# Kernel optimization log

Hardware: AMD Instinct MI355X
Metric: run time of the kernel (lower is better)

Reference implementation:

```python
import jax, jax.numpy as jnp
import numpy as np

BN_EPS = 1e-5


def _gather_neighbors(feat, idx):
    # feat: [B, N, C]; idx: [B, N, K] -> [B, N, K, C]
    B, N, C = feat.shape
    K = idx.shape[-1]
    g = jnp.take_along_axis(feat, idx.reshape(B, N * K)[:, :, None], axis=1)
    return g.reshape(B, N, K, C)


def setup_inputs() -> dict:
    key = jax.random.key(0)
    k1, k2, k3 = jax.random.split(key, 3)
    B, C, N, K, Cout = 4, 128, 4096, 16, 256
    x = jax.random.normal(k1, (B, C, N, 1), dtype=jnp.float32)
    edge_index = jax.random.randint(k2, (2, B, N, K), 0, N, dtype=jnp.int64)
    # 1x1 conv weight [Cout, 2C] (kaiming-like scale), bias zeros (per reset_parameters)
    fan_in = 2 * C
    w = jax.random.normal(k3, (Cout, 2 * C), dtype=jnp.float32) * np.sqrt(2.0 / fan_in)
    b = jnp.zeros((Cout,), dtype=jnp.float32)
    gamma = jnp.ones((Cout,), dtype=jnp.float32)
    beta = jnp.zeros((Cout,), dtype=jnp.float32)
    return {"x": x, "w": w, "b": b, "gamma": gamma, "beta": beta,
            "edge_index": edge_index}


def reference(x, w, b, gamma, beta, edge_index):
    # x: [B, C, N, 1], edge_index: [2, B, N, K]
    B, C, N, _ = x.shape
    feat = jnp.transpose(x[:, :, :, 0], (0, 2, 1))            # [B, N, C]
    x_i = _gather_neighbors(feat, edge_index[1])              # [B, N, K, C]
    x_j = _gather_neighbors(feat, edge_index[0])              # [B, N, K, C]
    h = jnp.concatenate([x_i, x_j - x_i], axis=-1)            # [B, N, K, 2C]
    # 1x1 conv == per-position matmul
    y = jnp.einsum('bnkc,oc->bnko', h, w) + b                 # [B, N, K, Cout]
    y = jax.nn.relu(y)
    # BatchNorm2d (train mode): biased stats over (B, N, K) per channel
    mean = jnp.mean(y, axis=(0, 1, 2))
    var = jnp.mean(jnp.square(y), axis=(0, 1, 2)) - jnp.square(mean)
    y = (y - mean) * jax.lax.rsqrt(var + BN_EPS) * gamma + beta
    # max over neighbors K, keepdim on last torch dim
    out = jnp.max(y, axis=2)                                  # [B, N, Cout]
    return jnp.transpose(out, (0, 2, 1))[:, :, :, None]       # [B, Cout, N, 1]
```

## Files before the change

### kernel.cpp

```cpp
#include <hip/hip_runtime.h>
#include <hip/hip_bf16.h>

#define BB 4
#define CC 128
#define TWOC 256
#define NN 4096
#define KK 16
#define COUT 256
#define BNK (BB*NN*KK)
#define NODES (BB*NN)

typedef __attribute__((ext_vector_type(8))) short short8;
typedef __attribute__((ext_vector_type(4))) float f32x4;

static __device__ __forceinline__ unsigned short f2bs(float f) {
  union { __hip_bfloat16 h; unsigned short s; } u;
  u.h = __float2bfloat16(f);
  return u.s;
}
static __device__ __forceinline__ float bs2f(unsigned short s) {
  union { unsigned int u; float f; } v;
  v.u = ((unsigned int)s) << 16;
  return v.f;
}

__global__ void __launch_bounds__(256) k0_prep(const float* __restrict__ x,
                                               unsigned short* __restrict__ featbf,
                                               const float* __restrict__ w,
                                               unsigned short* __restrict__ w12,
                                               float* __restrict__ gsum,
                                               float* __restrict__ gsq) {
  __shared__ float tile[64][129];
  int b = blockIdx.x >> 6;
  int n0 = (blockIdx.x & 63) << 6;
  int t = threadIdx.x;
  if (blockIdx.x == 0) { gsum[t] = 0.f; gsq[t] = 0.f; }
  {
    int flat = blockIdx.x * 256 + t;
    int col = flat >> 7, k = flat & 127;
    float v = (col < COUT) ? (w[col * TWOC + k] - w[col * TWOC + CC + k])
                           : w[(col - COUT) * TWOC + CC + k];
    w12[flat] = f2bs(v);
  }
#pragma unroll
  for (int i = 0; i < 32; ++i) {
    int flat = t + i * 256;
    int c = flat >> 6;
    int nl = flat & 63;
    tile[nl][c] = x[((size_t)(b * CC + c) * NN) + n0 + nl];
  }
  __syncthreads();
#pragma unroll
  for (int i = 0; i < 8; ++i) {
    int e = t + i * 256;
    int c4 = (e & 31) << 2;
    int nl = e >> 5;
    ushort4 u;
    u.x = f2bs(tile[nl][c4 + 0]);
    u.y = f2bs(tile[nl][c4 + 1]);
    u.z = f2bs(tile[nl][c4 + 2]);
    u.w = f2bs(tile[nl][c4 + 3]);
    *(ushort4*)(featbf + ((size_t)(b * NN + n0 + nl) * CC + c4)) = u;
  }
}

__global__ void __launch_bounds__(256, 4) k1_gemm(
    const unsigned short* __restrict__ featbf,
    const unsigned short* __restrict__ w12,
    unsigned short* __restrict__ Y)
{
  const int tid = threadIdx.x;
  const int wv   = tid >> 6;
  const int lane = tid & 63;
  const int l15  = lane & 15;
  const int lhi  = lane >> 4;
  const int bid  = blockIdx.x;
  const int b = (bid & 7) >> 1;
  const int inner = ((bid >> 3) << 1) | (bid & 1);
  const int rb = inner >> 2;
  const int cg = (inner & 3) * 4 + wv;
  const int colbase = cg * 32;
  const int row0 = b * NN + rb * 64;

  short8 wf[4][2];
#pragma unroll
  for (int t = 0; t < 4; ++t)
#pragma unroll
    for (int ct = 0; ct < 2; ++ct)
      wf[t][ct] = *(const short8*)(w12 + (size_t)(colbase + ct * 16 + l15) * CC + t * 32 + lhi * 8);

  short8 aA[4], aB[4];
#pragma unroll
  for (int t = 0; t < 4; ++t)
    aA[t] = *(const short8*)(featbf + (size_t)(row0 + l15) * CC + t * 32 + lhi * 8);

#pragma unroll
  for (int it = 0; it < 4; ++it) {
    short8* cur = (it & 1) ? aB : aA;
    short8* nxt = (it & 1) ? aA : aB;
    if (it < 3) {
      int r = row0 + (it + 1) * 16 + l15;
#pragma unroll
      for (int t = 0; t < 4; ++t)
        nxt[t] = *(const short8*)(featbf + (size_t)r * CC + t * 32 + lhi * 8);
    }
    f32x4 acc0 = {}, acc1 = {};
#pragma unroll
    for (int t = 0; t < 4; ++t) {
      acc0 = __builtin_amdgcn_mfma_f32_16x16x32_bf16(cur[t], wf[t][0], acc0, 0, 0, 0);
      acc1 = __builtin_amdgcn_mfma_f32_16x16x32_bf16(cur[t], wf[t][1], acc1, 0, 0, 0);
    }
    const int orow0 = row0 + it * 16;
#pragma unroll
    for (int i = 0; i < 4; ++i) {
      unsigned short* yr = Y + (size_t)(orow0 + lhi * 4 + i) * 512 + colbase + l15;
      yr[0]  = f2bs(acc0[i]);
      yr[16] = f2bs(acc1[i]);
    }
  }
}

__global__ void __launch_bounds__(256, 4) k2_edge(
    const unsigned short* __restrict__ Y,
    const float* __restrict__ bias,
    const int* __restrict__ eidx,
    unsigned short* __restrict__ nmaxh, unsigned short* __restrict__ nminh,
    float* __restrict__ gsum, float* __restrict__ gsq)
{
  __shared__ float sred[2][4][256];
  const int tid = threadIdx.x;
  const int wv   = tid >> 6;
  const int lane = tid & 63;
  const int bid  = blockIdx.x;
  const int b = (bid & 7) >> 1;
  const int inner = ((bid >> 3) << 1) | (bid & 1);
  const int nbase = b * NN + inner * 16 + wv * 4;
  const int c0 = lane * 4;

  const float bv0 = bias[c0], bv1 = bias[c0 + 1], bv2 = bias[c0 + 2], bv3 = bias[c0 + 3];
  const unsigned short* Yb = Y + (size_t)b * NN * 512;

  float ssum[4] = {0.f, 0.f, 0.f, 0.f};
  float ssq[4]  = {0.f, 0.f, 0.f, 0.f};

#pragma unroll
  for (int nn = 0; nn < 4; ++nn) {
    const int node = nbase + nn;
    const int* ej = eidx + (size_t)node * KK;
    const int* ei = ej + BNK;
    int4 ej4[4], ei4[4];
#pragma unroll
    for (int u = 0; u < 4; ++u) {
      ej4[u] = *(const int4*)(ej + u * 4);
      ei4[u] = *(const int4*)(ei + u * 4);
    }
    float mx[4] = {0.f, 0.f, 0.f, 0.f};
    float mn[4] = {1e30f, 1e30f, 1e30f, 1e30f};
#pragma unroll
    for (int e = 0; e < 16; ++e) {
      const int jj = ((const int*)ej4)[e];
      const int ii = ((const int*)ei4)[e];
      ushort4 uu = *(const ushort4*)(Yb + (size_t)ii * 512 + c0);
      ushort4 vv = *(const ushort4*)(Yb + (size_t)jj * 512 + 256 + c0);
      float y0 = fmaxf(bs2f(uu.x) + bs2f(vv.x) + bv0, 0.f);
      float y1 = fmaxf(bs2f(uu.y) + bs2f(vv.y) + bv1, 0.f);
      float y2 = fmaxf(bs2f(uu.z) + bs2f(vv.z) + bv2, 0.f);
      float y3 = fmaxf(bs2f(uu.w) + bs2f(vv.w) + bv3, 0.f);
      mx[0] = fmaxf(mx[0], y0); mn[0] = fminf(mn[0], y0); ssum[0] += y0; ssq[0] += y0 * y0;
      mx[1] = fmaxf(mx[1], y1); mn[1] = fminf(mn[1], y1); ssum[1] += y1; ssq[1] += y1 * y1;
      mx[2] = fmaxf(mx[2], y2); mn[2] = fminf(mn[2], y2); ssum[2] += y2; ssq[2] += y2 * y2;
      mx[3] = fmaxf(mx[3], y3); mn[3] = fminf(mn[3], y3); ssum[3] += y3; ssq[3] += y3 * y3;
    }
    ushort4 om, on;
    om.x = f2bs(mx[0]); om.y = f2bs(mx[1]); om.z = f2bs(mx[2]); om.w = f2bs(mx[3]);
    on.x = f2bs(mn[0]); on.y = f2bs(mn[1]); on.z = f2bs(mn[2]); on.w = f2bs(mn[3]);
    *(ushort4*)(nmaxh + (size_t)node * COUT + c0) = om;
    *(ushort4*)(nminh + (size_t)node * COUT + c0) = on;
  }

#pragma unroll
  for (int m = 0; m < 4; ++m) {
    sred[0][wv][c0 + m] = ssum[m];
    sred[1][wv][c0 + m] = ssq[m];
  }
  __syncthreads();
  {
    const int c = tid;
    float s = sred[0][0][c] + sred[0][1][c] + sred[0][2][c] + sred[0][3][c];
    float q = sred[1][0][c] + sred[1][1][c] + sred[1][2][c] + sred[1][3][c];
    atomicAdd(&gsum[c], s);
    atomicAdd(&gsq[c], q);
  }
}

__global__ void __launch_bounds__(256) k3_out(const unsigned short* __restrict__ nmaxh,
                                              const unsigned short* __restrict__ nminh,
                                              const float* __restrict__ gsum,
                                              const float* __restrict__ gsq,
                                              const float* __restrict__ gamma,
                                              const float* __restrict__ beta,
                                              float* __restrict__ out) {
  __shared__ float tile[COUT][33];
  int b = blockIdx.x >> 7;
  int n0 = (blockIdx.x & 127) << 5;
  int t = threadIdx.x;
  const float inv = 1.0f / (float)BNK;
  float mean = gsum[t] * inv;
  float var  = gsq[t] * inv - mean * mean;
  float sc = gamma[t] * rsqrtf(var + 1e-5f);
  float sh = beta[t] - mean * sc;
  const unsigned short* src = (sc >= 0.f) ? nmaxh : nminh;
#pragma unroll
  for (int rr = 0; rr < 32; ++rr) {
    size_t g = (size_t)(b * NN + n0 + rr) * COUT + t;
    tile[t][rr] = bs2f(src[g]) * sc + sh;
  }
  __syncthreads();
#pragma unroll
  for (int i = 0; i < 32; ++i) {
    int o = i * 8 + (t >> 5);
    int nl = t & 31;
    out[((size_t)(b * COUT + o) * NN) + n0 + nl] = tile[o][nl];
  }
}

extern "C" void kernel_launch(void* const* d_in, const int* in_sizes, int n_in,
                              void* d_out, int out_size, void* d_ws, size_t ws_size,
                              hipStream_t stream) {
  const float* x     = (const float*)d_in[0];
  const float* w     = (const float*)d_in[1];
  const float* bias  = (const float*)d_in[2];
  const float* gamma = (const float*)d_in[3];
  const float* beta  = (const float*)d_in[4];
  const int*   eidx  = (const int*)d_in[5];

  char* ws = (char*)d_ws;
  unsigned short* featbf = (unsigned short*)(ws);
  unsigned short* w12    = (unsigned short*)(ws + 4194304);
  unsigned short* nmaxh  = (unsigned short*)(ws);
  unsigned short* Ybuf   = (unsigned short*)(ws + 8388608);
  unsigned short* nminh  = (unsigned short*)(ws + 25165824);
  float* gsum = (float*)(ws + 33554432);
  float* gsq  = (float*)(ws + 33555456);
  float* out = (float*)d_out;

  k0_prep<<<256, 256, 0, stream>>>(x, featbf, w, w12, gsum, gsq);
  k1_gemm<<<1024, 256, 0, stream>>>(featbf, w12, Ybuf);
  k2_edge<<<1024, 256, 0, stream>>>(Ybuf, bias, eidx, nmaxh, nminh, gsum, gsq);
  k3_out<<<512, 256, 0, stream>>>(nmaxh, nminh, gsum, gsq, gamma, beta, out);
}
```

Baseline: 139.6 us.

## Split edge gather across more blocks, fold bias into GEMM, partition BN stat atomics

```diff
diff --git a/kernel.cpp b/kernel.cpp
--- a/kernel.cpp
+++ b/kernel.cpp
@@ -28,13 +28,12 @@
                                                unsigned short* __restrict__ featbf,
                                                const float* __restrict__ w,
                                                unsigned short* __restrict__ w12,
-                                               float* __restrict__ gsum,
-                                               float* __restrict__ gsq) {
+                                               float* __restrict__ gpart) {
   __shared__ float tile[64][129];
   int b = blockIdx.x >> 6;
   int n0 = (blockIdx.x & 63) << 6;
   int t = threadIdx.x;
-  if (blockIdx.x == 0) { gsum[t] = 0.f; gsq[t] = 0.f; }
+  if (blockIdx.x < 128) gpart[blockIdx.x * 256 + t] = 0.f;
   {
     int flat = blockIdx.x * 256 + t;
     int col = flat >> 7, k = flat & 127;
@@ -67,6 +66,7 @@
 __global__ void __launch_bounds__(256, 4) k1_gemm(
     const unsigned short* __restrict__ featbf,
     const unsigned short* __restrict__ w12,
+    const float* __restrict__ bias,
     unsigned short* __restrict__ Y)
 {
   const int tid = threadIdx.x;
@@ -89,6 +89,12 @@
     for (int ct = 0; ct < 2; ++ct)
       wf[t][ct] = *(const short8*)(w12 + (size_t)(colbase + ct * 16 + l15) * CC + t * 32 + lhi * 8);
 
+  float bv0 = 0.f, bv1 = 0.f;
+  if (colbase < COUT) {
+    bv0 = bias[colbase + l15];
+    bv1 = bias[colbase + 16 + l15];
+  }
+
   short8 aA[4], aB[4];
 #pragma unroll
   for (int t = 0; t < 4; ++t)
@@ -114,89 +120,91 @@
 #pragma unroll
     for (int i = 0; i < 4; ++i) {
       unsigned short* yr = Y + (size_t)(orow0 + lhi * 4 + i) * 512 + colbase + l15;
-      yr[0]  = f2bs(acc0[i]);
-      yr[16] = f2bs(acc1[i]);
+      yr[0]  = f2bs(acc0[i] + bv0);
+      yr[16] = f2bs(acc1[i] + bv1);
     }
   }
 }
 
-__global__ void __launch_bounds__(256, 4) k2_edge(
+__global__ void __launch_bounds__(256) k2_edge(
     const unsigned short* __restrict__ Y,
-    const float* __restrict__ bias,
     const int* __restrict__ eidx,
     unsigned short* __restrict__ nmaxh, unsigned short* __restrict__ nminh,
-    float* __restrict__ gsum, float* __restrict__ gsq)
+    float* __restrict__ gpart)
 {
-  __shared__ float sred[2][4][256];
-  const int tid = threadIdx.x;
+  __shared__ float smx[2][2][256];
+  __shared__ float smn[2][2][256];
+  __shared__ float ssm[2][2][256];
+  __shared__ float sq2[2][2][256];
+  const int tid  = threadIdx.x;
   const int wv   = tid >> 6;
   const int lane = tid & 63;
-  const int bid  = blockIdx.x;
-  const int b = (bid & 7) >> 1;
-  const int inner = ((bid >> 3) << 1) | (bid & 1);
-  const int nbase = b * NN + inner * 16 + wv * 4;
-  const int c0 = lane * 4;
-
-  const float bv0 = bias[c0], bv1 = bias[c0 + 1], bv2 = bias[c0 + 2], bv3 = bias[c0 + 3];
-  const unsigned short* Yb = Y + (size_t)b * NN * 512;
-
-  float ssum[4] = {0.f, 0.f, 0.f, 0.f};
-  float ssq[4]  = {0.f, 0.f, 0.f, 0.f};
-
-#pragma unroll
-  for (int nn = 0; nn < 4; ++nn) {
-    const int node = nbase + nn;
-    const int* ej = eidx + (size_t)node * KK;
-    const int* ei = ej + BNK;
-    int4 ej4[4], ei4[4];
-#pragma unroll
-    for (int u = 0; u < 4; ++u) {
-      ej4[u] = *(const int4*)(ej + u * 4);
-      ei4[u] = *(const int4*)(ei + u * 4);
-    }
-    float mx[4] = {0.f, 0.f, 0.f, 0.f};
-    float mn[4] = {1e30f, 1e30f, 1e30f, 1e30f};
-#pragma unroll
-    for (int e = 0; e < 16; ++e) {
-      const int jj = ((const int*)ej4)[e];
-      const int ii = ((const int*)ei4)[e];
-      ushort4 uu = *(const ushort4*)(Yb + (size_t)ii * 512 + c0);
-      ushort4 vv = *(const ushort4*)(Yb + (size_t)jj * 512 + 256 + c0);
-      float y0 = fmaxf(bs2f(uu.x) + bs2f(vv.x) + bv0, 0.f);
-      float y1 = fmaxf(bs2f(uu.y) + bs2f(vv.y) + bv1, 0.f);
-      float y2 = fmaxf(bs2f(uu.z) + bs2f(vv.z) + bv2, 0.f);
-      float y3 = fmaxf(bs2f(uu.w) + bs2f(vv.w) + bv3, 0.f);
-      mx[0] = fmaxf(mx[0], y0); mn[0] = fminf(mn[0], y0); ssum[0] += y0; ssq[0] += y0 * y0;
-      mx[1] = fmaxf(mx[1], y1); mn[1] = fminf(mn[1], y1); ssum[1] += y1; ssq[1] += y1 * y1;
-      mx[2] = fmaxf(mx[2], y2); mn[2] = fminf(mn[2], y2); ssum[2] += y2; ssq[2] += y2 * y2;
-      mx[3] = fmaxf(mx[3], y3); mn[3] = fminf(mn[3], y3); ssum[3] += y3; ssq[3] += y3 * y3;
-    }
-    ushort4 om, on;
-    om.x = f2bs(mx[0]); om.y = f2bs(mx[1]); om.z = f2bs(mx[2]); om.w = f2bs(mx[3]);
-    on.x = f2bs(mn[0]); on.y = f2bs(mn[1]); on.z = f2bs(mn[2]); on.w = f2bs(mn[3]);
-    *(ushort4*)(nmaxh + (size_t)node * COUT + c0) = om;
-    *(ushort4*)(nminh + (size_t)node * COUT + c0) = on;
-  }
-
+  const int ns   = wv >> 1;
+  const int hf   = wv & 1;
+  const int node = blockIdx.x * 2 + ns;
+  const int b    = node >> 12;
+  const int c0   = lane * 4;
+  const unsigned short* Yb = Y + ((size_t)b * NN) * 512;
+
+  const int* ej = eidx + (size_t)node * KK + hf * 8;
+  const int* ei = ej + BNK;
+  int4 ej0 = *(const int4*)(ej);
+  int4 ej1 = *(const int4*)(ej + 4);
+  int4 ei0 = *(const int4*)(ei);
+  int4 ei1 = *(const int4*)(ei + 4);
+  const int ejr[8] = {ej0.x, ej0.y, ej0.z, ej0.w, ej1.x, ej1.y, ej1.z, ej1.w};
+  const int eir[8] = {ei0.x, ei0.y, ei0.z, ei0.w, ei1.x, ei1.y, ei1.z, ei1.w};
+
+  ushort4 uu[8], vv[8];
+#pragma unroll
+  for (int e = 0; e < 8; ++e) {
+    uu[e] = *(const ushort4*)(Yb + (size_t)eir[e] * 512 + c0);
+    vv[e] = *(const ushort4*)(Yb + (size_t)ejr[e] * 512 + 256 + c0);
+  }
+
+  float mx[4] = {0.f, 0.f, 0.f, 0.f};
+  float mn[4] = {1e30f, 1e30f, 1e30f, 1e30f};
+  float sa[4] = {0.f, 0.f, 0.f, 0.f};
+  float sb[4] = {0.f, 0.f, 0.f, 0.f};
+#pragma unroll
+  for (int e = 0; e < 8; ++e) {
+    float y0 = fmaxf(bs2f(uu[e].x) + bs2f(vv[e].x), 0.f);
+    float y1 = fmaxf(bs2f(uu[e].y) + bs2f(vv[e].y), 0.f);
+    float y2 = fmaxf(bs2f(uu[e].z) + bs2f(vv[e].z), 0.f);
+    float y3 = fmaxf(bs2f(uu[e].w) + bs2f(vv[e].w), 0.f);
+    mx[0] = fmaxf(mx[0], y0); mn[0] = fminf(mn[0], y0); sa[0] += y0; sb[0] += y0 * y0;
+    mx[1] = fmaxf(mx[1], y1); mn[1] = fminf(mn[1], y1); sa[1] += y1; sb[1] += y1 * y1;
+    mx[2] = fmaxf(mx[2], y2); mn[2] = fminf(mn[2], y2); sa[2] += y2; sb[2] += y2 * y2;
+    mx[3] = fmaxf(mx[3], y3); mn[3] = fminf(mn[3], y3); sa[3] += y3; sb[3] += y3 * y3;
+  }
 #pragma unroll
   for (int m = 0; m < 4; ++m) {
-    sred[0][wv][c0 + m] = ssum[m];
-    sred[1][wv][c0 + m] = ssq[m];
+    smx[ns][hf][c0 + m] = mx[m];
+    smn[ns][hf][c0 + m] = mn[m];
+    ssm[ns][hf][c0 + m] = sa[m];
+    sq2[ns][hf][c0 + m] = sb[m];
   }
   __syncthreads();
-  {
-    const int c = tid;
-    float s = sred[0][0][c] + sred[0][1][c] + sred[0][2][c] + sred[0][3][c];
-    float q = sred[1][0][c] + sred[1][1][c] + sred[1][2][c] + sred[1][3][c];
-    atomicAdd(&gsum[c], s);
-    atomicAdd(&gsq[c], q);
-  }
+
+  const int c = tid;
+  float bsum = 0.f, bsq = 0.f;
+#pragma unroll
+  for (int k = 0; k < 2; ++k) {
+    float m0 = fmaxf(smx[k][0][c], smx[k][1][c]);
+    float n0 = fminf(smn[k][0][c], smn[k][1][c]);
+    nmaxh[(size_t)(blockIdx.x * 2 + k) * COUT + c] = f2bs(m0);
+    nminh[(size_t)(blockIdx.x * 2 + k) * COUT + c] = f2bs(n0);
+    bsum += ssm[k][0][c] + ssm[k][1][c];
+    bsq  += sq2[k][0][c] + sq2[k][1][c];
+  }
+  const int slot = blockIdx.x & 63;
+  atomicAdd(&gpart[slot * 256 + c], bsum);
+  atomicAdd(&gpart[16384 + slot * 256 + c], bsq);
 }
 
 __global__ void __launch_bounds__(256) k3_out(const unsigned short* __restrict__ nmaxh,
                                               const unsigned short* __restrict__ nminh,
-                                              const float* __restrict__ gsum,
-                                              const float* __restrict__ gsq,
+                                              const float* __restrict__ gpart,
                                               const float* __restrict__ gamma,
                                               const float* __restrict__ beta,
                                               float* __restrict__ out) {
@@ -204,9 +212,15 @@
   int b = blockIdx.x >> 7;
   int n0 = (blockIdx.x & 127) << 5;
   int t = threadIdx.x;
+  float s = 0.f, q = 0.f;
+#pragma unroll
+  for (int u = 0; u < 64; ++u) {
+    s += gpart[u * 256 + t];
+    q += gpart[16384 + u * 256 + t];
+  }
   const float inv = 1.0f / (float)BNK;
-  float mean = gsum[t] * inv;
-  float var  = gsq[t] * inv - mean * mean;
+  float mean = s * inv;
+  float var  = q * inv - mean * mean;
   float sc = gamma[t] * rsqrtf(var + 1e-5f);
   float sh = beta[t] - mean * sc;
   const unsigned short* src = (sc >= 0.f) ? nmaxh : nminh;
@@ -240,12 +254,11 @@
   unsigned short* nmaxh  = (unsigned short*)(ws);
   unsigned short* Ybuf   = (unsigned short*)(ws + 8388608);
   unsigned short* nminh  = (unsigned short*)(ws + 25165824);
-  float* gsum = (float*)(ws + 33554432);
-  float* gsq  = (float*)(ws + 33555456);
+  float* gpart = (float*)(ws + 33554432);
   float* out = (float*)d_out;
 
-  k0_prep<<<256, 256, 0, stream>>>(x, featbf, w, w12, gsum, gsq);
-  k1_gemm<<<1024, 256, 0, stream>>>(featbf, w12, Ybuf);
-  k2_edge<<<1024, 256, 0, stream>>>(Ybuf, bias, eidx, nmaxh, nminh, gsum, gsq);
-  k3_out<<<512, 256, 0, stream>>>(nmaxh, nminh, gsum, gsq, gamma, beta, out);
-}
+  k0_prep<<<256, 256, 0, stream>>>(x, featbf, w, w12, gpart);
+  k1_gemm<<<1024, 256, 0, stream>>>(featbf, w12, bias, Ybuf);
+  k2_edge<<<8192, 256, 0, stream>>>(Ybuf, eidx, nmaxh, nminh, gpart);
+  k3_out<<<512, 256, 0, stream>>>(nmaxh, nminh, gpart, gamma, beta, out);
+}
```

After: 128.1 us. 8.3% less time.
